# Kernel tuning notes

Measured on AMD Instinct MI355X. Metric: run time of the kernel, lower is better.

Reference implementation:

```python
import jax, jax.numpy as jnp
import numpy as np

B, N, IN_DIM, HID = 16, 2048, 128, 128
EPS = 1e-5


def _layer(x, W, b, g, beta):
    # x: (B, N, d_in) -> (B, N, HID)
    h = jnp.einsum('bnd,dh->bnh', x, W) + b
    mu = jnp.mean(h, axis=-1, keepdims=True)
    var = jnp.mean((h - mu) ** 2, axis=-1, keepdims=True)
    h = (h - mu) * jax.lax.rsqrt(var + EPS) * g + beta
    return jax.nn.relu(h)


def setup_inputs() -> dict:
    key = jax.random.key(0)
    ks = jax.random.split(key, 8)
    x = jax.random.normal(ks[0], (B, N, IN_DIM), dtype=jnp.float32)
    adj = jax.random.uniform(ks[1], (B, N, N), dtype=jnp.float32)
    inp = {'x': x, 'adj': adj}
    dims = [IN_DIM, HID, HID]
    for i in range(3):
        d_in = dims[i]
        scale = 1.0 / np.sqrt(d_in)
        inp[f'W{i}'] = jax.random.uniform(ks[2 + i], (d_in, HID), dtype=jnp.float32, minval=-scale, maxval=scale)
        inp[f'b{i}'] = jax.random.uniform(ks[5 + i], (HID,), dtype=jnp.float32, minval=-scale, maxval=scale)
        inp[f'g{i}'] = jnp.ones((HID,), dtype=jnp.float32)
        inp[f'be{i}'] = jnp.zeros((HID,), dtype=jnp.float32)
    return inp


def reference(x, adj, W0, b0, g0, be0, W1, b1, g1, be1, W2, b2, g2, be2):
    params = [(W0, b0, g0, be0), (W1, b1, g1, be1), (W2, b2, g2, be2)]
    h = x
    for (W, b, g, beta) in params:
        h_agg = jnp.einsum('bnm,bmd->bnd', adj, h)  # dense adjacency aggregation
        h = _layer(h_agg, W, b, g, beta)
    return h
```

## Files before the change

### kernel.cpp

```cpp
#include <hip/hip_runtime.h>
#include <hip/hip_bf16.h>

typedef __bf16 bf16;
typedef __bf16 bf16x8 __attribute__((ext_vector_type(8)));
typedef float  f32x4  __attribute__((ext_vector_type(4)));

static constexpr int NB  = 16;
static constexpr int NN  = 2048;
static constexpr int HID = 128;

__device__ __forceinline__ void gload_lds16(const bf16* g, bf16* l) {
    __builtin_amdgcn_global_load_lds(
        (const __attribute__((address_space(1))) unsigned int*)g,
        (__attribute__((address_space(3))) unsigned int*)l, 16, 0, 0);
}


__global__ __launch_bounds__(256) void prep_wt(const float* __restrict__ W0,
                                               const float* __restrict__ W1,
                                               const float* __restrict__ W2,
                                               bf16* __restrict__ WTg) {
    int l = blockIdx.x;
    const float* W = (l == 0) ? W0 : (l == 1) ? W1 : W2;
    bf16* out = WTg + l * 16384;
    int tid = threadIdx.x;
#pragma unroll
    for (int i = 0; i < 8; ++i) {
        int p = i * 256 + tid;
        int n = p >> 4, half = (p >> 3) & 1, cs = p & 7;
        int kc = cs ^ (n & 7);
        int kbase = half * 64 + kc * 8;
        bf16x8 o;
#pragma unroll
        for (int r = 0; r < 8; ++r) o[r] = (bf16)W[(kbase + r) * 128 + n];
        *(bf16x8*)(out + p * 8) = o;
    }
}

__global__ __launch_bounds__(256) void prep_xt(const float* __restrict__ x,
                                               bf16* __restrict__ xTt) {
    __shared__ bf16 T[128 * 136];
    const int blk = blockIdx.x;
    const int b = blk >> 4, node0 = (blk & 15) * 128;
    const int tid = threadIdx.x;
    const float* xb = x + ((size_t)b * NN + node0) * HID;
#pragma unroll
    for (int i = 0; i < 64; ++i) {
        int idx = i * 256 + tid;
        int node = idx >> 7, hid = idx & 127;
        T[hid * 136 + node] = (bf16)xb[(size_t)node * HID + hid];
    }
    __syncthreads();
#pragma unroll
    for (int i = 0; i < 8; ++i) {
        int p = i * 256 + tid;
        int half = p >> 10, p1 = p & 1023;
        int n = p1 >> 3, cs = p1 & 7, c = cs ^ (n & 7), m = half * 64 + c * 8;
        *(bf16x8*)(xTt + ((size_t)b * 32 + (node0 >> 6) + half) * 8192 + p1 * 8)
            = *(const bf16x8*)(T + n * 136 + m);
    }
}

template<bool FINAL>
__device__ __forceinline__ void epilogue(
        bf16* lds, const f32x4 (&acc)[2][4],
        const bf16* __restrict__ WTg,
        const float* __restrict__ bias, const float* __restrict__ gam,
        const float* __restrict__ bet, bf16* __restrict__ hOut,
        float* __restrict__ outF, int b, int mtile, int m0) {
    const int tid = threadIdx.x, wave = tid >> 6, lane = tid & 63;
    const int c0 = lane & 15, q = lane >> 4;
    const int wm = wave >> 1, wn = wave & 1;

    bf16* G = lds;
#pragma unroll
    for (int mt = 0; mt < 2; ++mt)
#pragma unroll
        for (int r = 0; r < 4; ++r) {
            int row = wm * 32 + mt * 16 + q * 4 + r;
#pragma unroll
            for (int nt = 0; nt < 4; ++nt) {
                int col = wn * 64 + nt * 16 + c0;
                G[row * 136 + col] = (bf16)acc[mt][nt][r];
            }
        }
    __syncthreads();

    f32x4 a2[8] = {};
    {
        const int gr = wave * 16 + c0;
#pragma unroll
        for (int ks = 0; ks < 4; ++ks) {
            bf16x8 af = *(const bf16x8*)(G + gr * 136 + ks * 32 + q * 8);
#pragma unroll
            for (int nt = 0; nt < 8; ++nt) {
                int n = nt * 16 + c0;
                int ch = n * 16 + (ks >> 1) * 8 + ((((ks & 1) << 2) | q) ^ (n & 7));
                bf16x8 bw = *(const bf16x8*)(WTg + (size_t)ch * 8);
                a2[nt] = __builtin_amdgcn_mfma_f32_16x16x32_bf16(af, bw, a2[nt], 0, 0, 0);
            }
        }
    }

    float bv[8], gv[8], ev[8];
#pragma unroll
    for (int nt = 0; nt < 8; ++nt) {
        int n = nt * 16 + c0;
        bv[nt] = bias[n]; gv[nt] = gam[n]; ev[nt] = bet[n];
    }
    bf16* Cs = lds;
    if constexpr (!FINAL) __syncthreads();
#pragma unroll
    for (int r = 0; r < 4; ++r) {
        float v[8], s1 = 0.f, s2 = 0.f;
#pragma unroll
        for (int nt = 0; nt < 8; ++nt) {
            float xv = a2[nt][r] + bv[nt];
            v[nt] = xv; s1 += xv; s2 += xv * xv;
        }
#pragma unroll
        for (int off = 1; off < 16; off <<= 1) {
            s1 += __shfl_xor(s1, off);
            s2 += __shfl_xor(s2, off);
        }
        float mu = s1 * (1.f / 128.f);
        float var = s2 * (1.f / 128.f) - mu * mu;
        float rs = rsqrtf(var + 1e-5f);
        int row = wave * 16 + q * 4 + r;
        if constexpr (FINAL) {
            size_t ro = ((size_t)b * NN + m0 + row) * HID;
#pragma unroll
            for (int nt = 0; nt < 8; ++nt) {
                float o = fmaxf((v[nt] - mu) * rs * gv[nt] + ev[nt], 0.f);
                outF[ro + nt * 16 + c0] = o;
            }
        } else {
#pragma unroll
            for (int nt = 0; nt < 8; ++nt) {
                float o = fmaxf((v[nt] - mu) * rs * gv[nt] + ev[nt], 0.f);
                Cs[(nt * 16 + c0) * 136 + row] = (bf16)o;
            }
        }
    }
    if constexpr (!FINAL) {
        __syncthreads();
#pragma unroll
        for (int i = 0; i < 4; ++i) {
            int p = i * 512 + tid;
            int half = p >> 10, p1 = p & 1023;
            int n = p1 >> 3, cs = p1 & 7, c = cs ^ (n & 7), m = half * 64 + c * 8;
            *(bf16x8*)(hOut + ((size_t)b * 32 + mtile * 2 + half) * 8192 + p1 * 8)
                = *(const bf16x8*)(Cs + n * 136 + m);
        }
    }
}

__global__ __launch_bounds__(512, 1) void layer0(
        const float* __restrict__ Af, bf16* __restrict__ adjT,
        const bf16* __restrict__ Bt, const bf16* __restrict__ WTg,
        const float* __restrict__ bias, const float* __restrict__ gam,
        const float* __restrict__ bet, bf16* __restrict__ hOut) {
    __shared__ __align__(16) bf16 lds[65536];

    const int tid = threadIdx.x, wave = tid >> 6, lane = tid & 63;
    const int c0 = lane & 15, q = lane >> 4;
    const int blk = blockIdx.x, xcd = blk & 7, jj = blk >> 3;
    const int b = xcd * 2 + (jj & 1);
    const int mtile = jj >> 1, m0 = mtile * 128;
    const int wm = wave >> 1, wn = wave & 1;

    const bf16* Btb = Bt + (size_t)b * 32 * 8192;
    bf16* Atl = adjT + ((size_t)b * 16 + mtile) * (size_t)32 * 8192;

    f32x4 acc[2][4] = {};

    auto stageB = [&](int buf, int t) {
#pragma unroll
        for (int j = 0; j < 4; ++j) {
            int cb = j * 512 + wave * 64;
            gload_lds16(Btb + (size_t)t * 16384 + (size_t)(cb + lane) * 8,
                        lds + buf * 32768 + 16384 + cb * 8);
        }
    };
    auto compute = [&](int buf) {
        const bf16* As = lds + buf * 32768;
        const bf16* Bs = As + 16384;
#pragma unroll
        for (int T = 0; T < 2; ++T)
#pragma unroll
            for (int ks = 0; ks < 2; ++ks) {
                bf16x8 af[2], bf_[4];
#pragma unroll
                for (int mt = 0; mt < 2; ++mt) {
                    int row = wm * 32 + mt * 16 + c0;
                    int cb = (ks * 4 + q) ^ (row & 7);
                    af[mt] = *(const bf16x8*)(As + T * 8192 + row * 64 + cb * 8);
                }
#pragma unroll
                for (int nt = 0; nt < 4; ++nt) {
                    int row = wn * 64 + nt * 16 + c0;
                    int cb = (ks * 4 + q) ^ (row & 7);
                    bf_[nt] = *(const bf16x8*)(Bs + T * 8192 + row * 64 + cb * 8);
                }
#pragma unroll
                for (int mt = 0; mt < 2; ++mt)
#pragma unroll
                    for (int nt = 0; nt < 4; ++nt)
                        acc[mt][nt] = __builtin_amdgcn_mfma_f32_16x16x32_bf16(
                            af[mt], bf_[nt], acc[mt][nt], 0, 0, 0);
            }
    };

    int g_row[4], g_cc[4];
#pragma unroll
    for (int j = 0; j < 4; ++j) {
        int gi = j * 512 + tid;
        g_row[j] = gi >> 4; g_cc[j] = gi & 15;
    }
    f32x4 va[4], vb[4];
    auto loadA = [&](int t) {
#pragma unroll
        for (int j = 0; j < 4; ++j) {
            const float* s = Af + (size_t)b * NN * NN
                           + (size_t)(m0 + g_row[j]) * NN + t * 128 + g_cc[j] * 8;
            va[j] = *(const f32x4*)s;
            vb[j] = *(const f32x4*)(s + 4);
        }
    };
    auto writeA = [&](int buf, int t) {
#pragma unroll
        for (int j = 0; j < 4; ++j) {
            bf16x8 o = {(bf16)va[j].x, (bf16)va[j].y, (bf16)va[j].z, (bf16)va[j].w,
                        (bf16)vb[j].x, (bf16)vb[j].y, (bf16)vb[j].z, (bf16)vb[j].w};
            int tile = g_cc[j] >> 3, kc = g_cc[j] & 7;
            int ch = g_row[j] * 8 + (kc ^ (g_row[j] & 7));
            *(bf16x8*)(lds + buf * 32768 + tile * 8192 + ch * 8) = o;
            *(bf16x8*)(Atl + (size_t)t * 16384 + (size_t)tile * 8192 + ch * 8) = o;
        }
    };

    loadA(0); stageB(0, 0); writeA(0, 0);
    __syncthreads();
    int cur = 0;
    for (int t = 0; t < 16; ++t) {
        if (t < 15) { loadA(t + 1); stageB(cur ^ 1, t + 1); }
        compute(cur);
        if (t < 15) writeA(cur ^ 1, t + 1);
        __syncthreads();
        cur ^= 1;
    }

    epilogue<false>(lds, acc, WTg, bias, gam, bet, hOut, nullptr, b, mtile, m0);
}

template<bool FINAL>
__global__ __launch_bounds__(512, 1) void layerK(
        const bf16* __restrict__ adjT, const bf16* __restrict__ Bt,
        const bf16* __restrict__ WTg,
        const float* __restrict__ bias, const float* __restrict__ gam,
        const float* __restrict__ bet, bf16* __restrict__ hOut,
        float* __restrict__ outF) {
    __shared__ __align__(16) bf16 lds[65536];

    const int tid = threadIdx.x, wave = tid >> 6, lane = tid & 63;
    const int c0 = lane & 15, q = lane >> 4;
    const int blk = blockIdx.x, xcd = blk & 7, jj = blk >> 3;
    const int b = xcd * 2 + (jj & 1);
    const int mtile = jj >> 1, m0 = mtile * 128;
    const int wm = wave >> 1, wn = wave & 1;

    const bf16* Btb = Bt + (size_t)b * 32 * 8192;
    const bf16* Atl = adjT + ((size_t)b * 16 + mtile) * (size_t)32 * 8192;

    f32x4 acc[2][4] = {};

    auto stageA = [&](int buf, int t) {
#pragma unroll
        for (int j = 0; j < 4; ++j) {
            int cb = j * 512 + wave * 64;
            gload_lds16(Atl + (size_t)t * 16384 + (size_t)(cb + lane) * 8,
                        lds + buf * 32768 + cb * 8);
        }
    };
    auto stageB = [&](int buf, int t) {
#pragma unroll
        for (int j = 0; j < 4; ++j) {
            int cb = j * 512 + wave * 64;
            gload_lds16(Btb + (size_t)t * 16384 + (size_t)(cb + lane) * 8,
                        lds + buf * 32768 + 16384 + cb * 8);
        }
    };
    auto compute = [&](int buf) {
        const bf16* As = lds + buf * 32768;
        const bf16* Bs = As + 16384;
#pragma unroll
        for (int T = 0; T < 2; ++T)
#pragma unroll
            for (int ks = 0; ks < 2; ++ks) {
                bf16x8 af[2], bf_[4];
#pragma unroll
                for (int mt = 0; mt < 2; ++mt) {
                    int row = wm * 32 + mt * 16 + c0;
                    int cb = (ks * 4 + q) ^ (row & 7);
                    af[mt] = *(const bf16x8*)(As + T * 8192 + row * 64 + cb * 8);
                }
#pragma unroll
                for (int nt = 0; nt < 4; ++nt) {
                    int row = wn * 64 + nt * 16 + c0;
                    int cb = (ks * 4 + q) ^ (row & 7);
                    bf_[nt] = *(const bf16x8*)(Bs + T * 8192 + row * 64 + cb * 8);
                }
#pragma unroll
                for (int mt = 0; mt < 2; ++mt)
#pragma unroll
                    for (int nt = 0; nt < 4; ++nt)
                        acc[mt][nt] = __builtin_amdgcn_mfma_f32_16x16x32_bf16(
                            af[mt], bf_[nt], acc[mt][nt], 0, 0, 0);
            }
    };

    stageA(0, 0); stageB(0, 0);
    __syncthreads();
    int cur = 0;
    for (int t = 0; t < 16; ++t) {
        if (t < 15) { stageA(cur ^ 1, t + 1); stageB(cur ^ 1, t + 1); }
        compute(cur);
        __syncthreads();
        cur ^= 1;
    }

    epilogue<FINAL>(lds, acc, WTg, bias, gam, bet, hOut, outF, b, mtile, m0);
}

extern "C" void kernel_launch(void* const* d_in, const int* in_sizes, int n_in,
                              void* d_out, int out_size, void* d_ws, size_t ws_size,
                              hipStream_t stream) {
    const float* x   = (const float*)d_in[0];
    const float* adj = (const float*)d_in[1];
    const float* W[3]  = {(const float*)d_in[2],  (const float*)d_in[6],  (const float*)d_in[10]};
    const float* bb[3] = {(const float*)d_in[3],  (const float*)d_in[7],  (const float*)d_in[11]};
    const float* gg[3] = {(const float*)d_in[4],  (const float*)d_in[8],  (const float*)d_in[12]};
    const float* be[3] = {(const float*)d_in[5],  (const float*)d_in[9],  (const float*)d_in[13]};

    char* ws = (char*)d_ws;
    size_t off = 0;
    auto alloc = [&](size_t bytes) {
        char* p = ws + off; off = (off + bytes + 255) & ~(size_t)255; return p;
    };
    bf16* WTg  = (bf16*)alloc((size_t)3 * 16384 * 2);
    bf16* xTt  = (bf16*)alloc((size_t)NB * 32 * 8192 * 2);
    bf16* hT0  = (bf16*)alloc((size_t)NB * 32 * 8192 * 2);
    bf16* hT1  = (bf16*)alloc((size_t)NB * 32 * 8192 * 2);
    bf16* adjT = (bf16*)alloc((size_t)NB * 16 * 32 * 8192 * 2);

    float* outF = (float*)d_out;

    prep_wt<<<3, 256, 0, stream>>>(W[0], W[1], W[2], WTg);
    prep_xt<<<256, 256, 0, stream>>>(x, xTt);

    layer0<<<256, 512, 0, stream>>>(adj, adjT, xTt, WTg,
                                    bb[0], gg[0], be[0], hT0);
    layerK<false><<<256, 512, 0, stream>>>(adjT, hT0, WTg + 16384,
                                           bb[1], gg[1], be[1], hT1, nullptr);
    layerK<true ><<<256, 512, 0, stream>>>(adjT, hT1, WTg + 2 * 16384,
                                           bb[2], gg[2], be[2], nullptr, outF);
}
```

Before: 497.6 us.

## Store adjacency in MFMA fragment order and load A directly to registers

Layer 0 now writes the bf16 adjacency copy in a per-wave MFMA fragment layout, so layers 1 and 2 can load A operands straight from global memory into registers instead of staging them through LDS. Each wave owns 16 rows across all 128 output columns (8 accumulators). Only B is staged in LDS, in larger K chunks, under a manually unrolled pipeline with explicit vmcnt waits and sched barriers. A new epilogue matches this wave layout. This removes LDS traffic and barriers for A, at the cost of more register pressure and reliance on the hand-tuned wait counts being correct.

```diff
diff --git a/kernel.cpp b/kernel.cpp
--- a/kernel.cpp
+++ b/kernel.cpp
@@ -14,6 +14,9 @@
         (const __attribute__((address_space(1))) unsigned int*)g,
         (__attribute__((address_space(3))) unsigned int*)l, 16, 0, 0);
 }
+
+#define WAITV(n) asm volatile("s_waitcnt vmcnt(" #n ")" ::: "memory")
+#define SCHEDB() __builtin_amdgcn_sched_barrier(0)
 
 
 __global__ __launch_bounds__(256) void prep_wt(const float* __restrict__ W0,
@@ -62,7 +65,7 @@
 }
 
 template<bool FINAL>
-__device__ __forceinline__ void epilogue(
+__device__ __forceinline__ void epilogue24(
         bf16* lds, const f32x4 (&acc)[2][4],
         const bf16* __restrict__ WTg,
         const float* __restrict__ bias, const float* __restrict__ gam,
@@ -155,8 +158,97 @@
     }
 }
 
+template<bool FINAL>
+__device__ __forceinline__ void epilogue8(
+        bf16* lds, const f32x4 (&acc)[8],
+        const bf16* __restrict__ WTg,
+        const float* __restrict__ bias, const float* __restrict__ gam,
+        const float* __restrict__ bet, bf16* __restrict__ hOut,
+        float* __restrict__ outF, int b, int mtile, int m0) {
+    const int tid = threadIdx.x, wave = tid >> 6, lane = tid & 63;
+    const int c0 = lane & 15, q = lane >> 4;
+
+    bf16* G = lds;
+#pragma unroll
+    for (int nt = 0; nt < 8; ++nt)
+#pragma unroll
+        for (int r = 0; r < 4; ++r) {
+            int row = wave * 16 + q * 4 + r;
+            G[row * 136 + nt * 16 + c0] = (bf16)acc[nt][r];
+        }
+    __syncthreads();
+
+    f32x4 a2[8] = {};
+    {
+        const int gr = wave * 16 + c0;
+#pragma unroll
+        for (int ks = 0; ks < 4; ++ks) {
+            bf16x8 af = *(const bf16x8*)(G + gr * 136 + ks * 32 + q * 8);
+#pragma unroll
+            for (int nt = 0; nt < 8; ++nt) {
+                int n = nt * 16 + c0;
+                int ch = n * 16 + (ks >> 1) * 8 + ((((ks & 1) << 2) | q) ^ (n & 7));
+                bf16x8 bw = *(const bf16x8*)(WTg + (size_t)ch * 8);
+                a2[nt] = __builtin_amdgcn_mfma_f32_16x16x32_bf16(af, bw, a2[nt], 0, 0, 0);
+            }
+        }
+    }
+
+    float bv[8], gv[8], ev[8];
+#pragma unroll
+    for (int nt = 0; nt < 8; ++nt) {
+        int n = nt * 16 + c0;
+        bv[nt] = bias[n]; gv[nt] = gam[n]; ev[nt] = bet[n];
+    }
+    bf16* Cs = lds;
+    if constexpr (!FINAL) __syncthreads();
+#pragma unroll
+    for (int r = 0; r < 4; ++r) {
+        float v[8], s1 = 0.f, s2 = 0.f;
+#pragma unroll
+        for (int nt = 0; nt < 8; ++nt) {
+            float xv = a2[nt][r] + bv[nt];
+            v[nt] = xv; s1 += xv; s2 += xv * xv;
+        }
+#pragma unroll
+        for (int off = 1; off < 16; off <<= 1) {
+            s1 += __shfl_xor(s1, off);
+            s2 += __shfl_xor(s2, off);
+        }
+        float mu = s1 * (1.f / 128.f);
+        float var = s2 * (1.f / 128.f) - mu * mu;
+        float rs = rsqrtf(var + 1e-5f);
+        int row = wave * 16 + q * 4 + r;
+        if constexpr (FINAL) {
+            size_t ro = ((size_t)b * NN + m0 + row) * HID;
+#pragma unroll
+            for (int nt = 0; nt < 8; ++nt) {
+                float o = fmaxf((v[nt] - mu) * rs * gv[nt] + ev[nt], 0.f);
+                outF[ro + nt * 16 + c0] = o;
+            }
+        } else {
+#pragma unroll
+            for (int nt = 0; nt < 8; ++nt) {
+                float o = fmaxf((v[nt] - mu) * rs * gv[nt] + ev[nt], 0.f);
+                Cs[(nt * 16 + c0) * 136 + row] = (bf16)o;
+            }
+        }
+    }
+    if constexpr (!FINAL) {
+        __syncthreads();
+#pragma unroll
+        for (int i = 0; i < 4; ++i) {
+            int p = i * 512 + tid;
+            int half = p >> 10, p1 = p & 1023;
+            int n = p1 >> 3, cs = p1 & 7, c = cs ^ (n & 7), m = half * 64 + c * 8;
+            *(bf16x8*)(hOut + ((size_t)b * 32 + mtile * 2 + half) * 8192 + p1 * 8)
+                = *(const bf16x8*)(Cs + n * 136 + m);
+        }
+    }
+}
+
 __global__ __launch_bounds__(512, 1) void layer0(
-        const float* __restrict__ Af, bf16* __restrict__ adjT,
+        const float* __restrict__ Af, bf16* __restrict__ adjFr,
         const bf16* __restrict__ Bt, const bf16* __restrict__ WTg,
         const float* __restrict__ bias, const float* __restrict__ gam,
         const float* __restrict__ bet, bf16* __restrict__ hOut) {
@@ -170,7 +262,7 @@
     const int wm = wave >> 1, wn = wave & 1;
 
     const bf16* Btb = Bt + (size_t)b * 32 * 8192;
-    bf16* Atl = adjT + ((size_t)b * 16 + mtile) * (size_t)32 * 8192;
+    bf16* Afr = adjFr + ((size_t)b * 16 + mtile) * (size_t)8 * 32768;
 
     f32x4 acc[2][4] = {};
 
@@ -235,7 +327,9 @@
             int tile = g_cc[j] >> 3, kc = g_cc[j] & 7;
             int ch = g_row[j] * 8 + (kc ^ (g_row[j] & 7));
             *(bf16x8*)(lds + buf * 32768 + tile * 8192 + ch * 8) = o;
-            *(bf16x8*)(Atl + (size_t)t * 16384 + (size_t)tile * 8192 + ch * 8) = o;
+            int wf = g_row[j] >> 4, c0f = g_row[j] & 15;
+            int sf = t * 4 + (g_cc[j] >> 2), qf = g_cc[j] & 3;
+            *(bf16x8*)(Afr + (size_t)wf * 32768 + sf * 512 + (qf * 16 + c0f) * 8) = o;
         }
     };
 
@@ -250,12 +344,12 @@
         cur ^= 1;
     }
 
-    epilogue<false>(lds, acc, WTg, bias, gam, bet, hOut, nullptr, b, mtile, m0);
+    epilogue24<false>(lds, acc, WTg, bias, gam, bet, hOut, nullptr, b, mtile, m0);
 }
 
 template<bool FINAL>
-__global__ __launch_bounds__(512, 1) void layerK(
-        const bf16* __restrict__ adjT, const bf16* __restrict__ Bt,
+__global__ __launch_bounds__(512, 1) void layerW(
+        const bf16* __restrict__ adjFr, const bf16* __restrict__ Bt,
         const bf16* __restrict__ WTg,
         const float* __restrict__ bias, const float* __restrict__ gam,
         const float* __restrict__ bet, bf16* __restrict__ hOut,
@@ -267,69 +361,58 @@
     const int blk = blockIdx.x, xcd = blk & 7, jj = blk >> 3;
     const int b = xcd * 2 + (jj & 1);
     const int mtile = jj >> 1, m0 = mtile * 128;
-    const int wm = wave >> 1, wn = wave & 1;
 
     const bf16* Btb = Bt + (size_t)b * 32 * 8192;
-    const bf16* Atl = adjT + ((size_t)b * 16 + mtile) * (size_t)32 * 8192;
-
-    f32x4 acc[2][4] = {};
-
-    auto stageA = [&](int buf, int t) {
-#pragma unroll
-        for (int j = 0; j < 4; ++j) {
-            int cb = j * 512 + wave * 64;
-            gload_lds16(Atl + (size_t)t * 16384 + (size_t)(cb + lane) * 8,
-                        lds + buf * 32768 + cb * 8);
-        }
-    };
-    auto stageB = [&](int buf, int t) {
-#pragma unroll
-        for (int j = 0; j < 4; ++j) {
-            int cb = j * 512 + wave * 64;
-            gload_lds16(Btb + (size_t)t * 16384 + (size_t)(cb + lane) * 8,
-                        lds + buf * 32768 + 16384 + cb * 8);
-        }
-    };
-    auto compute = [&](int buf) {
-        const bf16* As = lds + buf * 32768;
-        const bf16* Bs = As + 16384;
-#pragma unroll
-        for (int T = 0; T < 2; ++T)
-#pragma unroll
-            for (int ks = 0; ks < 2; ++ks) {
-                bf16x8 af[2], bf_[4];
-#pragma unroll
-                for (int mt = 0; mt < 2; ++mt) {
-                    int row = wm * 32 + mt * 16 + c0;
-                    int cb = (ks * 4 + q) ^ (row & 7);
-                    af[mt] = *(const bf16x8*)(As + T * 8192 + row * 64 + cb * 8);
-                }
-#pragma unroll
-                for (int nt = 0; nt < 4; ++nt) {
-                    int row = wn * 64 + nt * 16 + c0;
-                    int cb = (ks * 4 + q) ^ (row & 7);
-                    bf_[nt] = *(const bf16x8*)(Bs + T * 8192 + row * 64 + cb * 8);
-                }
-#pragma unroll
-                for (int mt = 0; mt < 2; ++mt)
-#pragma unroll
-                    for (int nt = 0; nt < 4; ++nt)
-                        acc[mt][nt] = __builtin_amdgcn_mfma_f32_16x16x32_bf16(
-                            af[mt], bf_[nt], acc[mt][nt], 0, 0, 0);
-            }
-    };
-
-    stageA(0, 0); stageB(0, 0);
+    const bf16* Aw  = adjFr + (((size_t)b * 16 + mtile) * 8 + wave) * 32768;
+
+    f32x4 acc[8] = {};
+    bf16x8 aE[8], aO[8];
+
+#define ISSUE_B(CH) do {                                                      \
+    _Pragma("unroll") for (int j = 0; j < 8; ++j) {                           \
+        int cb = j * 512 + wave * 64;                                         \
+        gload_lds16(Btb + (size_t)(CH) * 32768 + (size_t)(cb + lane) * 8,     \
+                    lds + ((CH) & 1) * 32768 + cb * 8);                       \
+    } SCHEDB(); } while (0)
+
+#define ISSUE_A(DST, CH) do {                                                 \
+    _Pragma("unroll") for (int s = 0; s < 8; ++s)                             \
+        DST[s] = *(const bf16x8*)(Aw + ((CH) * 8 + s) * 512 + lane * 8);      \
+    SCHEDB(); } while (0)
+
+#define STEPS(CH, CUR) do {                                                   \
+    const bf16* Bs_ = lds + ((CH) & 1) * 32768;                               \
+    _Pragma("unroll") for (int s = 0; s < 8; ++s) {                           \
+        const bf16* Bt_ = Bs_ + (s >> 1) * 8192;                              \
+        int kb = (s & 1) * 4 + q;                                             \
+        _Pragma("unroll") for (int nt = 0; nt < 8; ++nt) {                    \
+            int row = nt * 16 + c0;                                           \
+            bf16x8 bw = *(const bf16x8*)(Bt_ + row * 64 + (kb ^ (row & 7)) * 8); \
+            acc[nt] = __builtin_amdgcn_mfma_f32_16x16x32_bf16(                \
+                CUR[s], bw, acc[nt], 0, 0, 0);                                \
+        }                                                                     \
+    } } while (0)
+
+    ISSUE_B(0);
+    ISSUE_A(aE, 0);
+    WAITV(8);
+    __builtin_amdgcn_s_barrier();
+
+    ISSUE_B(1); ISSUE_A(aO, 1); STEPS(0, aE); WAITV(8); __builtin_amdgcn_s_barrier();
+    ISSUE_B(2); ISSUE_A(aE, 2); STEPS(1, aO); WAITV(8); __builtin_amdgcn_s_barrier();
+    ISSUE_B(3); ISSUE_A(aO, 3); STEPS(2, aE); WAITV(8); __builtin_amdgcn_s_barrier();
+    ISSUE_B(4); ISSUE_A(aE, 4); STEPS(3, aO); WAITV(8); __builtin_amdgcn_s_barrier();
+    ISSUE_B(5); ISSUE_A(aO, 5); STEPS(4, aE); WAITV(8); __builtin_amdgcn_s_barrier();
+    ISSUE_B(6); ISSUE_A(aE, 6); STEPS(5, aO); WAITV(8); __builtin_amdgcn_s_barrier();
+    ISSUE_B(7); ISSUE_A(aO, 7); STEPS(6, aE); WAITV(8); __builtin_amdgcn_s_barrier();
+    STEPS(7, aO);
+
+#undef ISSUE_B
+#undef ISSUE_A
+#undef STEPS
+
     __syncthreads();
-    int cur = 0;
-    for (int t = 0; t < 16; ++t) {
-        if (t < 15) { stageA(cur ^ 1, t + 1); stageB(cur ^ 1, t + 1); }
-        compute(cur);
-        __syncthreads();
-        cur ^= 1;
-    }
-
-    epilogue<FINAL>(lds, acc, WTg, bias, gam, bet, hOut, outF, b, mtile, m0);
+    epilogue8<FINAL>(lds, acc, WTg, bias, gam, bet, hOut, outF, b, mtile, m0);
 }
 
 extern "C" void kernel_launch(void* const* d_in, const int* in_sizes, int n_in,
@@ -347,21 +430,21 @@
     auto alloc = [&](size_t bytes) {
         char* p = ws + off; off = (off + bytes + 255) & ~(size_t)255; return p;
     };
-    bf16* WTg  = (bf16*)alloc((size_t)3 * 16384 * 2);
-    bf16* xTt  = (bf16*)alloc((size_t)NB * 32 * 8192 * 2);
-    bf16* hT0  = (bf16*)alloc((size_t)NB * 32 * 8192 * 2);
-    bf16* hT1  = (bf16*)alloc((size_t)NB * 32 * 8192 * 2);
-    bf16* adjT = (bf16*)alloc((size_t)NB * 16 * 32 * 8192 * 2);
+    bf16* WTg   = (bf16*)alloc((size_t)3 * 16384 * 2);
+    bf16* xTt   = (bf16*)alloc((size_t)NB * 32 * 8192 * 2);
+    bf16* hT0   = (bf16*)alloc((size_t)NB * 32 * 8192 * 2);
+    bf16* hT1   = (bf16*)alloc((size_t)NB * 32 * 8192 * 2);
+    bf16* adjFr = (bf16*)alloc((size_t)NB * 16 * 8 * 32768 * 2);
 
     float* outF = (float*)d_out;
 
     prep_wt<<<3, 256, 0, stream>>>(W[0], W[1], W[2], WTg);
     prep_xt<<<256, 256, 0, stream>>>(x, xTt);
 
-    layer0<<<256, 512, 0, stream>>>(adj, adjT, xTt, WTg,
+    layer0<<<256, 512, 0, stream>>>(adj, adjFr, xTt, WTg,
                                     bb[0], gg[0], be[0], hT0);
-    layerK<false><<<256, 512, 0, stream>>>(adjT, hT0, WTg + 16384,
+    layerW<false><<<256, 512, 0, stream>>>(adjFr, hT0, WTg + 16384,
                                            bb[1], gg[1], be[1], hT1, nullptr);
-    layerK<true ><<<256, 512, 0, stream>>>(adjT, hT1, WTg + 2 * 16384,
+    layerW<true ><<<256, 512, 0, stream>>>(adjFr, hT1, WTg + 2 * 16384,
                                            bb[2], gg[2], be[2], nullptr, outF);
 }
```

Measured after the change: 501.2 us. Within noise of the previous version (+0.7%).
